# Optimization experiments

Hardware: AMD Instinct MI355X
Metric: run time of the kernel (lower is better)

## Reference

```python
import jax, jax.numpy as jnp
import numpy as np

N = 32768      # total nodes
E = 262144     # total edges (avg degree 8)
S = 128        # graph segments
B = 16         # batch entries
C = S // B     # segments per batch entry
NF, NC = 90, 36
OP, OD = 120, 64
D0, DX, GIN, GH = 190, 380, 256, 512


def setup_inputs() -> dict:
    key = jax.random.key(0)
    ks = jax.random.split(key, 16)
    rn = lambda k, shape, s=0.02: jax.random.normal(k, shape, jnp.float32) * s
    return {
        "node_features": jax.random.normal(ks[0], (N, NF), jnp.float32),
        "node_config_features": jax.random.normal(ks[1], (N, NC), jnp.float32),
        "emb_table": rn(ks[2], (OP, OD), 1.0),
        "w1": rn(ks[3], (DX, D0)), "b1": jnp.zeros((DX,), jnp.float32),
        "g1": jnp.ones((DX,), jnp.float32), "be1": jnp.zeros((DX,), jnp.float32),
        "w2": rn(ks[4], (GIN, DX)), "b2": jnp.zeros((GIN,), jnp.float32),
        "g2": jnp.ones((GIN,), jnp.float32), "be2": jnp.zeros((GIN,), jnp.float32),
        "wl1": rn(ks[5], (GH, GIN)), "bl1": jnp.zeros((GH,), jnp.float32), "wr1": rn(ks[6], (GH, GIN)),
        "wl2": rn(ks[7], (GH, GH)), "bl2": jnp.zeros((GH,), jnp.float32), "wr2": rn(ks[8], (GH, GH)),
        "wl3": rn(ks[9], (GH, GH)), "bl3": jnp.zeros((GH,), jnp.float32), "wr3": rn(ks[10], (GH, GH)),
        "wc": rn(ks[11], (1, GH)), "bc": jnp.zeros((1,), jnp.float32),
        "node_ops": jax.random.randint(ks[12], (N,), 0, OP),
        "edges": jax.random.randint(ks[13], (2, E), 0, N),
        # cumulative end indices, equal-size segments; batches = segment -> batch entry
        "node_separation": (jnp.arange(S, dtype=jnp.int32) + 1) * (N // S),
        "batches": jnp.repeat(jnp.arange(B, dtype=jnp.int32), C),
    }


def _leaky(x):
    return jnp.where(x >= 0, x, 0.01 * x)


def _graphwise_ln(x, seg_id, counts, gamma, beta):
    # per-graph-segment mean/var over all nodes and features, per-feature affine
    D = x.shape[1]
    s = jax.ops.segment_sum(jnp.sum(x, -1), seg_id, num_segments=S)
    ss = jax.ops.segment_sum(jnp.sum(x * x, -1), seg_id, num_segments=S)
    cnt = counts.astype(x.dtype) * D
    mean = s / cnt
    var = ss / cnt - mean * mean
    inv = jax.lax.rsqrt(var + 1e-5)
    return (x - mean[seg_id, None]) * inv[seg_id, None] * gamma + beta


def _pairnorm(x):
    # PyG PairNorm, scale=1: center over nodes, divide by sqrt(mean row norm^2)
    xc = x - jnp.mean(x, axis=0, keepdims=True)
    denom = 1e-5 + jnp.sqrt(jnp.mean(jnp.sum(xc * xc, -1)))
    return xc / denom


def _sage(x, src, dst, inv_deg, wl, bl, wr):
    # SAGEConv(mean): lin_l(mean_neighbors) + lin_r(x)
    agg = jax.ops.segment_sum(x[src], dst, num_segments=N) * inv_deg[:, None]
    return agg @ wl.T + bl + x @ wr.T


def reference(node_features, node_config_features, emb_table, w1, b1, g1, be1,
              w2, b2, g2, be2, wl1, bl1, wr1, wl2, bl2, wr2, wl3, bl3, wr3,
              wc, bc, node_ops, edges, node_separation, batches):
    seg_id = jnp.searchsorted(node_separation, jnp.arange(N), side="right")
    counts = jnp.diff(node_separation, prepend=0)
    src, dst = edges[0], edges[1]
    deg = jax.ops.segment_sum(jnp.ones((E,), jnp.float32), dst, num_segments=N)
    inv_deg = 1.0 / jnp.maximum(deg, 1.0)

    x = jnp.concatenate([node_features, node_config_features, emb_table[node_ops]], axis=1)
    # node_features_mlp: Linear -> LeakyReLU -> GLN -> Linear -> LeakyReLU -> GLN
    x = _graphwise_ln(_leaky(x @ w1.T + b1), seg_id, counts, g1, be1)
    x = _graphwise_ln(_leaky(x @ w2.T + b2), seg_id, counts, g2, be2)
    # GraphSAGE: 3 layers, PairNorm + ReLU after all but the last
    x = jax.nn.relu(_pairnorm(_sage(x, src, dst, inv_deg, wl1, bl1, wr1)))
    x = jax.nn.relu(_pairnorm(_sage(x, src, dst, inv_deg, wl2, bl2, wr2)))
    x = _sage(x, src, dst, inv_deg, wl3, bl3, wr3)
    # ragged per-segment sum pooling (replaces the python loop) -> [S, GH]
    seg_sums = jax.ops.segment_sum(x, seg_id, num_segments=S)
    # batches = repeat(arange(B), C) and segments are in order -> reshape groups
    agg = seg_sums.reshape(B, C, GH)
    out = agg @ wc.T + bc  # [B, C, 1]
    return jnp.squeeze(out, 2)
```

## Files before the change

kernel.cpp:

```cpp
#include <hip/hip_runtime.h>
#include <hip/hip_bf16.h>

#define NN   32768
#define EE   262144
#define SS   128
#define NF_  90
#define NC_  36
#define OD_  64
#define D0_  190
#define DX_  380
#define GIN_ 256
#define GH_  512

typedef __attribute__((ext_vector_type(8))) short  s8v;
typedef __attribute__((ext_vector_type(4))) float  f4v;

typedef const __attribute__((address_space(1))) void* gas_ptr;
typedef __attribute__((address_space(3))) void*       las_ptr;

__device__ __forceinline__ float bf2f(unsigned short u) {
  return __uint_as_float(((unsigned)u) << 16);
}
__device__ __forceinline__ unsigned short f2bf(float f) {
  unsigned u = __float_as_uint(f);
  u += 0x7FFFu + ((u >> 16) & 1u);
  return (unsigned short)(u >> 16);
}

__global__ void deg_count(const int* __restrict__ dst, int* __restrict__ deg) {
  int e = blockIdx.x * 256 + threadIdx.x;
  if (e < EE) atomicAdd(&deg[dst[e]], 1);
}

__global__ void inv_deg_k(const int* __restrict__ deg, float* __restrict__ inv_deg) {
  int n = blockIdx.x * 256 + threadIdx.x;
  if (n < NN) inv_deg[n] = 1.0f / fmaxf((float)deg[n], 1.0f);
}

__global__ __launch_bounds__(256) void blk_sum_k(const int* __restrict__ deg,
                                                 int* __restrict__ bsum) {
  __shared__ int buf[256];
  int tid = threadIdx.x;
  buf[tid] = deg[blockIdx.x * 256 + tid];
  __syncthreads();
  for (int off = 128; off > 0; off >>= 1) {
    if (tid < off) buf[tid] += buf[tid + off];
    __syncthreads();
  }
  if (tid == 0) bsum[blockIdx.x] = buf[0];
}

__global__ __launch_bounds__(128) void blk_scan_k(const int* __restrict__ bsum,
                                                  int* __restrict__ boff) {
  __shared__ int buf[128];
  int tid = threadIdx.x;
  int v = bsum[tid];
  buf[tid] = v;
  __syncthreads();
  for (int d = 1; d < 128; d <<= 1) {
    int t = (tid >= d) ? buf[tid - d] : 0;
    __syncthreads();
    if (tid >= d) buf[tid] += t;
    __syncthreads();
  }
  boff[tid] = buf[tid] - v;
}

__global__ __launch_bounds__(256) void offsets_k(const int* __restrict__ deg,
                                                 const int* __restrict__ boff,
                                                 int* __restrict__ offsets) {
  __shared__ int buf[256];
  int tid = threadIdx.x;
  int i = blockIdx.x * 256 + tid;
  int v = deg[i];
  buf[tid] = v;
  __syncthreads();
  for (int d = 1; d < 256; d <<= 1) {
    int t = (tid >= d) ? buf[tid - d] : 0;
    __syncthreads();
    if (tid >= d) buf[tid] += t;
    __syncthreads();
  }
  offsets[i] = boff[blockIdx.x] + buf[tid] - v;
  if (i == 0) offsets[NN] = EE;
}

__global__ void bucket_k(const int* __restrict__ src, const int* __restrict__ dst,
                         const int* __restrict__ offsets, int* __restrict__ cursor,
                         int* __restrict__ srcs) {
  int e = blockIdx.x * 256 + threadIdx.x;
  if (e < EE) {
    int d = dst[e];
    int pos = offsets[d] + atomicAdd(&cursor[d], 1);
    srcs[pos] = src[e];
  }
}

#define CW1  73728
#define CW2  172032
#define CWL1 303104
#define CWR1 434176
#define CWL2 696320
#define CWR2 958464
#define CWL3 1220608
#define CWR3 1482752

__global__ void conv_all(const float* __restrict__ w1, const float* __restrict__ w2,
                         const float* __restrict__ wl1, const float* __restrict__ wr1,
                         const float* __restrict__ wl2, const float* __restrict__ wr2,
                         const float* __restrict__ wl3, const float* __restrict__ wr3,
                         unsigned short* __restrict__ w1b, unsigned short* __restrict__ w2b,
                         unsigned short* __restrict__ wl1b, unsigned short* __restrict__ wr1b,
                         unsigned short* __restrict__ wl2b, unsigned short* __restrict__ wr2b,
                         unsigned short* __restrict__ wl3b, unsigned short* __restrict__ wr3b) {
  int idx = blockIdx.x * 256 + threadIdx.x;
  if (idx >= CWR3) return;
  if (idx < CW1) {
    int r = idx / 192, c = idx - r * 192;
    w1b[idx] = f2bf((r < DX_ && c < D0_) ? w1[r * D0_ + c] : 0.0f);
  } else if (idx < CW2) {
    int i = idx - CW1;
    int r = i / 384, c = i - r * 384;
    w2b[i] = f2bf((c < DX_) ? w2[r * DX_ + c] : 0.0f);
  } else if (idx < CWL1) { int i = idx - CW2;  wl1b[i] = f2bf(wl1[i]); }
  else if (idx < CWR1)   { int i = idx - CWL1; wr1b[i] = f2bf(wr1[i]); }
  else if (idx < CWL2)   { int i = idx - CWR1; wl2b[i] = f2bf(wl2[i]); }
  else if (idx < CWR2)   { int i = idx - CWL2; wr2b[i] = f2bf(wr2[i]); }
  else if (idx < CWL3)   { int i = idx - CWR2; wl3b[i] = f2bf(wl3[i]); }
  else                   { int i = idx - CWL3; wr3b[i] = f2bf(wr3[i]); }
}

__global__ void build_x0_bf16(const float* __restrict__ nf, const float* __restrict__ ncf,
                              const float* __restrict__ emb, const int* __restrict__ ops,
                              unsigned short* __restrict__ x0) {
  int idx = blockIdx.x * 256 + threadIdx.x;
  if (idx >= NN * 192) return;
  int n = idx / 192;
  int c = idx - n * 192;
  float v;
  if (c < NF_)            v = nf[n * NF_ + c];
  else if (c < NF_ + NC_) v = ncf[n * NC_ + (c - NF_)];
  else if (c < D0_)       v = emb[ops[n] * OD_ + (c - (NF_ + NC_))];
  else                    v = 0.0f;
  x0[idx] = f2bf(v);
}

__device__ __forceinline__ void stage_tile_async(const unsigned short* __restrict__ G, int ld,
                                                 int base_row, int k0,
                                                 unsigned short* __restrict__ lds, int tid) {
#pragma unroll
  for (int i = 0; i < 2; ++i) {
    int c = tid + i * 256;
    int row = c & 127;
    int off = c >> 7;
    const unsigned short* src = G + (size_t)(base_row + row) * ld + k0 + off * 8;
    unsigned short* dst = lds + off * 1024 + row * 8;
    __builtin_amdgcn_global_load_lds((gas_ptr)(const void*)src, (las_ptr)(void*)dst,
                                     16, 0, 0);
  }
}

__global__ __launch_bounds__(256) void mfma_gemm2(
    const unsigned short* __restrict__ A1, int lda1,
    const unsigned short* __restrict__ B1, int ldb1, int K1,
    const unsigned short* __restrict__ A2, int lda2,
    const unsigned short* __restrict__ B2, int ldb2, int K2,
    const float* __restrict__ bias,
    float* __restrict__ C, int ldc, int Nreal, int mode, int swz,
    float* __restrict__ st0, float* __restrict__ st1,
    const float* __restrict__ wcp, float* __restrict__ outp)
{
  __shared__ unsigned short As[4096];
  __shared__ unsigned short Bs[4096];
  __shared__ float red[256];
  __shared__ float cs[128], css[128];
  int tid = threadIdx.x;
  int lane = tid & 63;
  int w = tid >> 6;
  int wm = (w & 1) * 64;
  int wn = (w >> 1) * 64;
  int bm, bn;
  if (swz) {
    int L = blockIdx.x;
    int xcd = L & 7;
    int s = L >> 3;
    bn = (s & 3) * 128;
    bm = ((s >> 2) * 8 + xcd) * 128;
  } else {
    bm = blockIdx.y * 128;
    bn = blockIdx.x * 128;
  }
  int quad = lane >> 4;
  int r16 = lane & 15;

  f4v acc[4][4] = {};

#pragma unroll 1
  for (int ph = 0; ph < 2; ++ph) {
    const unsigned short* A = ph ? A2 : A1;
    const unsigned short* B = ph ? B2 : B1;
    int lda = ph ? lda2 : lda1;
    int ldb = ph ? ldb2 : ldb1;
    int K = ph ? K2 : K1;
    for (int k0 = 0; k0 < K; k0 += 32) {
      stage_tile_async(A, lda, bm, k0, As, tid);
      stage_tile_async(B, ldb, bn, k0, Bs, tid);
      __syncthreads();
      s8v af[4], bfr[4];
#pragma unroll
      for (int mi = 0; mi < 4; ++mi)
        af[mi] = *(const s8v*)&As[quad * 1024 + (wm + mi * 16 + r16) * 8];
#pragma unroll
      for (int ni = 0; ni < 4; ++ni)
        bfr[ni] = *(const s8v*)&Bs[quad * 1024 + (wn + ni * 16 + r16) * 8];
#pragma unroll
      for (int mi = 0; mi < 4; ++mi)
#pragma unroll
        for (int ni = 0; ni < 4; ++ni)
          acc[mi][ni] = __builtin_amdgcn_mfma_f32_16x16x32_bf16(
              af[mi], bfr[ni], acc[mi][ni], 0, 0, 0);
      __syncthreads();
    }
  }

  int seg = bm >> 8;

  if (mode == 1) {
    float lsum = 0.0f, lssq = 0.0f;
#pragma unroll
    for (int mi = 0; mi < 4; ++mi) {
      int gm = bm + wm + mi * 16 + quad * 4;
#pragma unroll
      for (int ni = 0; ni < 4; ++ni) {
        int gn = bn + wn + ni * 16 + r16;
        if (gn < Nreal) {
          float bv = bias[gn];
#pragma unroll
          for (int r = 0; r < 4; ++r) {
            float v = acc[mi][ni][r] + bv;
            v = (v >= 0.0f) ? v : 0.01f * v;
            C[(size_t)(gm + r) * ldc + gn] = v;
            lsum += v;
            lssq += v * v;
          }
        }
      }
    }
    red[tid] = lsum;
    __syncthreads();
    for (int off = 128; off > 0; off >>= 1) {
      if (tid < off) red[tid] += red[tid + off];
      __syncthreads();
    }
    if (tid == 0) atomicAdd(&st0[seg], red[0]);
    __syncthreads();
    red[tid] = lssq;
    __syncthreads();
    for (int off = 128; off > 0; off >>= 1) {
      if (tid < off) red[tid] += red[tid + off];
      __syncthreads();
    }
    if (tid == 0) atomicAdd(&st1[seg], red[0]);
  } else if (mode == 2) {
    if (tid < 128) { cs[tid] = 0.0f; css[tid] = 0.0f; }
    __syncthreads();
#pragma unroll
    for (int ni = 0; ni < 4; ++ni) {
      int col = wn + ni * 16 + r16;
      int gn = bn + col;
      float bv = bias[gn];
      float psum = 0.0f, pssq = 0.0f;
#pragma unroll
      for (int mi = 0; mi < 4; ++mi) {
        int gm = bm + wm + mi * 16 + quad * 4;
#pragma unroll
        for (int r = 0; r < 4; ++r) {
          float v = acc[mi][ni][r] + bv;
          C[(size_t)(gm + r) * ldc + gn] = v;
          psum += v;
          pssq += v * v;
        }
      }
      atomicAdd(&cs[col], psum);
      atomicAdd(&css[col], pssq);
    }
    __syncthreads();
    if (tid < 128) {
      atomicAdd(&st0[bn + tid], cs[tid]);
      atomicAdd(&st1[bn + tid], css[tid]);
    }
  } else {
    float part = 0.0f;
#pragma unroll
    for (int ni = 0; ni < 4; ++ni) {
      int gn = bn + wn + ni * 16 + r16;
      float bv = bias[gn];
      float wv = wcp[gn];
      float colsum = 0.0f;
#pragma unroll
      for (int mi = 0; mi < 4; ++mi)
#pragma unroll
        for (int r = 0; r < 4; ++r)
          colsum += acc[mi][ni][r] + bv;
      part += colsum * wv;
    }
    red[tid] = part;
    __syncthreads();
    for (int off = 128; off > 0; off >>= 1) {
      if (tid < off) red[tid] += red[tid + off];
      __syncthreads();
    }
    if (tid == 0) atomicAdd(&outp[seg], red[0]);
  }
}

__global__ __launch_bounds__(256) void gln_apply_bf16(
    const float* __restrict__ x, int ld, int D, int Dp,
    const float* __restrict__ seg_sum, const float* __restrict__ seg_ssq,
    const float* __restrict__ g, const float* __restrict__ be,
    unsigned short* __restrict__ out) {
  int r = blockIdx.x;
  int s = r >> 8;
  float cnt = 256.0f * (float)D;
  float m = seg_sum[s] / cnt;
  float var = seg_ssq[s] / cnt - m * m;
  float inv = rsqrtf(var + 1e-5f);
  const float* row = x + (size_t)r * ld;
  unsigned short* orow = out + (size_t)r * Dp;
  for (int c = threadIdx.x; c < Dp; c += 256) {
    float v = (c < D) ? ((row[c] - m) * inv * g[c] + be[c]) : 0.0f;
    orow[c] = f2bf(v);
  }
}

__global__ __launch_bounds__(256) void aggregate4(const unsigned short* __restrict__ x,
                                                  int D4log,
                                                  unsigned short* __restrict__ agg,
                                                  const int* __restrict__ offsets,
                                                  const int* __restrict__ srcs,
                                                  const float* __restrict__ inv_deg) {
  int tid = threadIdx.x;
  int D4 = 1 << D4log;
  int npb = 256 >> D4log;
  int n = blockIdx.x * npb + (tid >> D4log);
  int f4 = tid & (D4 - 1);
  int start = offsets[n], end = offsets[n + 1];
  float wgt = inv_deg[n];
  const uint2* xb = (const uint2*)x;
  float a0 = 0.0f, a1 = 0.0f, a2 = 0.0f, a3 = 0.0f;
  for (int e = start; e < end; ++e) {
    uint2 v = xb[((size_t)srcs[e] << D4log) + f4];
    a0 += bf2f((unsigned short)(v.x & 0xffffu));
    a1 += bf2f((unsigned short)(v.x >> 16));
    a2 += bf2f((unsigned short)(v.y & 0xffffu));
    a3 += bf2f((unsigned short)(v.y >> 16));
  }
  uint2 o;
  o.x = ((unsigned)f2bf(a1 * wgt) << 16) | (unsigned)f2bf(a0 * wgt);
  o.y = ((unsigned)f2bf(a3 * wgt) << 16) | (unsigned)f2bf(a2 * wgt);
  ((uint2*)agg)[((size_t)n << D4log) + f4] = o;
}

__global__ __launch_bounds__(512) void pn_finalize(const float* __restrict__ colsum,
                                                   const float* __restrict__ colssq,
                                                   float* __restrict__ mu,
                                                   float* __restrict__ invd) {
  int f = threadIdx.x;
  float m = colsum[f] / (float)NN;
  mu[f] = m;
  float t = colssq[f] / (float)NN - m * m;
  __shared__ float buf[512];
  buf[f] = t;
  __syncthreads();
  for (int off = 256; off > 0; off >>= 1) {
    if (f < off) buf[f] += buf[f + off];
    __syncthreads();
  }
  if (f == 0) invd[0] = 1.0f / (1e-5f + sqrtf(fmaxf(buf[0], 0.0f)));
}

__global__ __launch_bounds__(128) void pn_apply_v(const float* __restrict__ y,
                                                  const float* __restrict__ mu,
                                                  const float* __restrict__ invd,
                                                  unsigned short* __restrict__ xb) {
  int r = blockIdx.x;
  int f4 = threadIdx.x;
  float id = invd[0];
  float4 v = ((const float4*)(y + (size_t)r * GH_))[f4];
  float4 m = ((const float4*)mu)[f4];
  float v0 = fmaxf((v.x - m.x) * id, 0.0f);
  float v1 = fmaxf((v.y - m.y) * id, 0.0f);
  float v2 = fmaxf((v.z - m.z) * id, 0.0f);
  float v3 = fmaxf((v.w - m.w) * id, 0.0f);
  uint2 o;
  o.x = ((unsigned)f2bf(v1) << 16) | (unsigned)f2bf(v0);
  o.y = ((unsigned)f2bf(v3) << 16) | (unsigned)f2bf(v2);
  ((uint2*)(xb + (size_t)r * GH_))[f4] = o;
}

__global__ void init_out(float* __restrict__ out, const float* __restrict__ bc) {
  int s = threadIdx.x;
  if (s < SS) out[s] = bc[0];
}

extern "C" void kernel_launch(void* const* d_in, const int* in_sizes, int n_in,
                              void* d_out, int out_size, void* d_ws, size_t ws_size,
                              hipStream_t stream) {
  const float* node_features = (const float*)d_in[0];
  const float* node_config   = (const float*)d_in[1];
  const float* emb_table     = (const float*)d_in[2];
  const float* w1  = (const float*)d_in[3];
  const float* b1  = (const float*)d_in[4];
  const float* g1  = (const float*)d_in[5];
  const float* be1 = (const float*)d_in[6];
  const float* w2  = (const float*)d_in[7];
  const float* b2  = (const float*)d_in[8];
  const float* g2  = (const float*)d_in[9];
  const float* be2 = (const float*)d_in[10];
  const float* wl1 = (const float*)d_in[11];
  const float* bl1 = (const float*)d_in[12];
  const float* wr1 = (const float*)d_in[13];
  const float* wl2 = (const float*)d_in[14];
  const float* bl2 = (const float*)d_in[15];
  const float* wr2 = (const float*)d_in[16];
  const float* wl3 = (const float*)d_in[17];
  const float* bl3 = (const float*)d_in[18];
  const float* wr3 = (const float*)d_in[19];
  const float* wc  = (const float*)d_in[20];
  const float* bc  = (const float*)d_in[21];
  const int* node_ops = (const int*)d_in[22];
  const int* edges    = (const int*)d_in[23];
  float* out = (float*)d_out;

  char* ws = (char*)d_ws;
  size_t off = 0;
  auto alloc = [&](size_t bytes) -> void* {
    void* p = ws + off;
    off += (bytes + 255) & ~(size_t)255;
    return p;
  };

  int*   deg_i   = (int*)alloc(NN * 4);
  int*   cursor  = (int*)alloc(NN * 4);
  int*   offsets = (int*)alloc((NN + 1) * 4);
  int*   srcs    = (int*)alloc(EE * 4);
  int*   bsum    = (int*)alloc(SS * 4);
  int*   boff    = (int*)alloc(SS * 4);
  float* inv_deg = (float*)alloc(NN * 4);
  float* seg_sum = (float*)alloc(SS * 4);
  float* seg_ssq = (float*)alloc(SS * 4);
  float* colsum  = (float*)alloc(512 * 4);
  float* colssq  = (float*)alloc(512 * 4);
  float* mu      = (float*)alloc(512 * 4);
  float* invd    = (float*)alloc(256);
  unsigned short* w1b  = (unsigned short*)alloc((size_t)384 * 192 * 2);
  unsigned short* w2b  = (unsigned short*)alloc((size_t)256 * 384 * 2);
  unsigned short* wl1b = (unsigned short*)alloc((size_t)512 * 256 * 2);
  unsigned short* wr1b = (unsigned short*)alloc((size_t)512 * 256 * 2);
  unsigned short* wl2b = (unsigned short*)alloc((size_t)512 * 512 * 2);
  unsigned short* wr2b = (unsigned short*)alloc((size_t)512 * 512 * 2);
  unsigned short* wl3b = (unsigned short*)alloc((size_t)512 * 512 * 2);
  unsigned short* wr3b = (unsigned short*)alloc((size_t)512 * 512 * 2);
  float*          Y    = (float*)alloc((size_t)NN * 512 * 4);
  unsigned short* BF1  = (unsigned short*)alloc((size_t)NN * 512 * 2);
  unsigned short* BF2  = (unsigned short*)alloc((size_t)NN * 512 * 2);
  unsigned short* BF3  = (unsigned short*)alloc((size_t)NN * 512 * 2);

  const int* esrc = edges;
  const int* edst = edges + EE;

  hipMemsetAsync(deg_i, 0, NN * 4, stream);
  hipMemsetAsync(cursor, 0, NN * 4, stream);
  deg_count<<<EE / 256, 256, 0, stream>>>(edst, deg_i);
  blk_sum_k<<<NN / 256, 256, 0, stream>>>(deg_i, bsum);
  blk_scan_k<<<1, 128, 0, stream>>>(bsum, boff);
  offsets_k<<<NN / 256, 256, 0, stream>>>(deg_i, boff, offsets);
  inv_deg_k<<<NN / 256, 256, 0, stream>>>(deg_i, inv_deg);
  bucket_k<<<EE / 256, 256, 0, stream>>>(esrc, edst, offsets, cursor, srcs);

  conv_all<<<(CWR3 + 255) / 256, 256, 0, stream>>>(w1, w2, wl1, wr1, wl2, wr2, wl3, wr3,
                                                   w1b, w2b, wl1b, wr1b, wl2b, wr2b,
                                                   wl3b, wr3b);

  init_out<<<1, SS, 0, stream>>>(out, bc);

  build_x0_bf16<<<(NN * 192 + 255) / 256, 256, 0, stream>>>(node_features, node_config,
                                                            emb_table, node_ops, BF1);
  hipMemsetAsync(seg_sum, 0, 1024, stream);
  {
    dim3 g(384 / 128, NN / 128);
    mfma_gemm2<<<g, 256, 0, stream>>>(BF1, 192, w1b, 192, 192,
                                      nullptr, 0, nullptr, 0, 0,
                                      b1, Y, 384, DX_, 1, 0,
                                      seg_sum, seg_ssq, nullptr, nullptr);
  }
  gln_apply_bf16<<<NN, 256, 0, stream>>>(Y, 384, DX_, 384, seg_sum, seg_ssq, g1, be1, BF2);

  hipMemsetAsync(seg_sum, 0, 1024, stream);
  {
    dim3 g(256 / 128, NN / 128);
    mfma_gemm2<<<g, 256, 0, stream>>>(BF2, 384, w2b, 384, 384,
                                      nullptr, 0, nullptr, 0, 0,
                                      b2, Y, 256, GIN_, 1, 0,
                                      seg_sum, seg_ssq, nullptr, nullptr);
  }
  gln_apply_bf16<<<NN, 256, 0, stream>>>(Y, 256, GIN_, 256, seg_sum, seg_ssq, g2, be2, BF3);

  aggregate4<<<NN / 4, 256, 0, stream>>>(BF3, 6, BF1, offsets, srcs, inv_deg);
  hipMemsetAsync(colsum, 0, 4096, stream);
  mfma_gemm2<<<1024, 256, 0, stream>>>(BF1, 256, wl1b, 256, 256,
                                       BF3, 256, wr1b, 256, 256,
                                       bl1, Y, 512, GH_, 2, 1,
                                       colsum, colssq, nullptr, nullptr);
  pn_finalize<<<1, 512, 0, stream>>>(colsum, colssq, mu, invd);
  pn_apply_v<<<NN, 128, 0, stream>>>(Y, mu, invd, BF2);

  aggregate4<<<NN / 2, 256, 0, stream>>>(BF2, 7, BF1, offsets, srcs, inv_deg);
  hipMemsetAsync(colsum, 0, 4096, stream);
  mfma_gemm2<<<1024, 256, 0, stream>>>(BF1, 512, wl2b, 512, 512,
                                       BF2, 512, wr2b, 512, 512,
                                       bl2, Y, 512, GH_, 2, 1,
                                       colsum, colssq, nullptr, nullptr);
  pn_finalize<<<1, 512, 0, stream>>>(colsum, colssq, mu, invd);
  pn_apply_v<<<NN, 128, 0, stream>>>(Y, mu, invd, BF3);

  aggregate4<<<NN / 2, 256, 0, stream>>>(BF3, 7, BF1, offsets, srcs, inv_deg);
  mfma_gemm2<<<1024, 256, 0, stream>>>(BF1, 512, wl3b, 512, 512,
                                       BF3, 512, wr3b, 512, 512,
                                       bl3, nullptr, 512, GH_, 3, 1,
                                       nullptr, nullptr, wc, out);
}
```

Before: 663.7 us.

## Merge prep kernels and memsets, widen aggregation to 16-byte loads, reuse LDS

Merges weight conversion, input building, output init and stat zeroing into one grid-stride prep kernel. The inverse-degree computation moves into the offsets kernel, and the two degree/cursor memsets become one, assuming the two buffers are contiguous. The neighbour aggregation now loads eight bf16 values per thread as uint4 instead of four, and the GEMM reuses its staging LDS for the reduction scratch, which cuts LDS use. These changes mainly remove launches and memsets and reduce gather instruction count, at the cost of relying on buffer adjacency.

```diff
diff --git a/kernel.cpp b/kernel.cpp
--- a/kernel.cpp
+++ b/kernel.cpp
@@ -18,23 +18,21 @@
 typedef const __attribute__((address_space(1))) void* gas_ptr;
 typedef __attribute__((address_space(3))) void*       las_ptr;
 
-__device__ __forceinline__ float bf2f(unsigned short u) {
-  return __uint_as_float(((unsigned)u) << 16);
+__device__ __forceinline__ float bf2f(unsigned u) {
+  return __uint_as_float(u << 16);
 }
 __device__ __forceinline__ unsigned short f2bf(float f) {
   unsigned u = __float_as_uint(f);
   u += 0x7FFFu + ((u >> 16) & 1u);
   return (unsigned short)(u >> 16);
 }
+__device__ __forceinline__ unsigned pack2(float a, float b) {
+  return ((unsigned)f2bf(b) << 16) | (unsigned)f2bf(a);
+}
 
 __global__ void deg_count(const int* __restrict__ dst, int* __restrict__ deg) {
   int e = blockIdx.x * 256 + threadIdx.x;
   if (e < EE) atomicAdd(&deg[dst[e]], 1);
-}
-
-__global__ void inv_deg_k(const int* __restrict__ deg, float* __restrict__ inv_deg) {
-  int n = blockIdx.x * 256 + threadIdx.x;
-  if (n < NN) inv_deg[n] = 1.0f / fmaxf((float)deg[n], 1.0f);
 }
 
 __global__ __launch_bounds__(256) void blk_sum_k(const int* __restrict__ deg,
@@ -68,7 +66,8 @@
 
 __global__ __launch_bounds__(256) void offsets_k(const int* __restrict__ deg,
                                                  const int* __restrict__ boff,
-                                                 int* __restrict__ offsets) {
+                                                 int* __restrict__ offsets,
+                                                 float* __restrict__ inv_deg) {
   __shared__ int buf[256];
   int tid = threadIdx.x;
   int i = blockIdx.x * 256 + tid;
@@ -82,6 +81,7 @@
     __syncthreads();
   }
   offsets[i] = boff[blockIdx.x] + buf[tid] - v;
+  inv_deg[i] = 1.0f / fmaxf((float)v, 1.0f);
   if (i == 0) offsets[NN] = EE;
 }
 
@@ -105,44 +105,50 @@
 #define CWL3 1220608
 #define CWR3 1482752
 
-__global__ void conv_all(const float* __restrict__ w1, const float* __restrict__ w2,
-                         const float* __restrict__ wl1, const float* __restrict__ wr1,
-                         const float* __restrict__ wl2, const float* __restrict__ wr2,
-                         const float* __restrict__ wl3, const float* __restrict__ wr3,
-                         unsigned short* __restrict__ w1b, unsigned short* __restrict__ w2b,
-                         unsigned short* __restrict__ wl1b, unsigned short* __restrict__ wr1b,
-                         unsigned short* __restrict__ wl2b, unsigned short* __restrict__ wr2b,
-                         unsigned short* __restrict__ wl3b, unsigned short* __restrict__ wr3b) {
-  int idx = blockIdx.x * 256 + threadIdx.x;
-  if (idx >= CWR3) return;
-  if (idx < CW1) {
-    int r = idx / 192, c = idx - r * 192;
-    w1b[idx] = f2bf((r < DX_ && c < D0_) ? w1[r * D0_ + c] : 0.0f);
-  } else if (idx < CW2) {
-    int i = idx - CW1;
-    int r = i / 384, c = i - r * 384;
-    w2b[i] = f2bf((c < DX_) ? w2[r * DX_ + c] : 0.0f);
-  } else if (idx < CWL1) { int i = idx - CW2;  wl1b[i] = f2bf(wl1[i]); }
-  else if (idx < CWR1)   { int i = idx - CWL1; wr1b[i] = f2bf(wr1[i]); }
-  else if (idx < CWL2)   { int i = idx - CWR1; wl2b[i] = f2bf(wl2[i]); }
-  else if (idx < CWR2)   { int i = idx - CWL2; wr2b[i] = f2bf(wr2[i]); }
-  else if (idx < CWL3)   { int i = idx - CWR2; wl3b[i] = f2bf(wl3[i]); }
-  else                   { int i = idx - CWL3; wr3b[i] = f2bf(wr3[i]); }
-}
-
-__global__ void build_x0_bf16(const float* __restrict__ nf, const float* __restrict__ ncf,
-                              const float* __restrict__ emb, const int* __restrict__ ops,
-                              unsigned short* __restrict__ x0) {
-  int idx = blockIdx.x * 256 + threadIdx.x;
-  if (idx >= NN * 192) return;
-  int n = idx / 192;
-  int c = idx - n * 192;
-  float v;
-  if (c < NF_)            v = nf[n * NF_ + c];
-  else if (c < NF_ + NC_) v = ncf[n * NC_ + (c - NF_)];
-  else if (c < D0_)       v = emb[ops[n] * OD_ + (c - (NF_ + NC_))];
-  else                    v = 0.0f;
-  x0[idx] = f2bf(v);
+__global__ __launch_bounds__(256) void prep_all(
+    const float* __restrict__ nf, const float* __restrict__ ncf,
+    const float* __restrict__ emb, const int* __restrict__ ops,
+    const float* __restrict__ w1, const float* __restrict__ w2,
+    const float* __restrict__ wl1, const float* __restrict__ wr1,
+    const float* __restrict__ wl2, const float* __restrict__ wr2,
+    const float* __restrict__ wl3, const float* __restrict__ wr3,
+    unsigned short* __restrict__ w1b, unsigned short* __restrict__ w2b,
+    unsigned short* __restrict__ wl1b, unsigned short* __restrict__ wr1b,
+    unsigned short* __restrict__ wl2b, unsigned short* __restrict__ wr2b,
+    unsigned short* __restrict__ wl3b, unsigned short* __restrict__ wr3b,
+    unsigned short* __restrict__ x0,
+    float* __restrict__ stat_all, float* __restrict__ outp,
+    const float* __restrict__ bc)
+{
+  const int T = 4096 * 256;
+  int gidx = blockIdx.x * 256 + threadIdx.x;
+  for (int i = gidx; i < 2560; i += T) stat_all[i] = 0.0f;
+  if (gidx < SS) outp[gidx] = bc[0];
+  for (int i = gidx; i < CWR3; i += T) {
+    if (i < CW1) {
+      int r = i / 192, c = i - r * 192;
+      w1b[i] = f2bf((r < DX_ && c < D0_) ? w1[r * D0_ + c] : 0.0f);
+    } else if (i < CW2) {
+      int j = i - CW1;
+      int r = j / 384, c = j - r * 384;
+      w2b[j] = f2bf((c < DX_) ? w2[r * DX_ + c] : 0.0f);
+    } else if (i < CWL1) { int j = i - CW2;  wl1b[j] = f2bf(wl1[j]); }
+    else if (i < CWR1)   { int j = i - CWL1; wr1b[j] = f2bf(wr1[j]); }
+    else if (i < CWL2)   { int j = i - CWR1; wl2b[j] = f2bf(wl2[j]); }
+    else if (i < CWR2)   { int j = i - CWL2; wr2b[j] = f2bf(wr2[j]); }
+    else if (i < CWL3)   { int j = i - CWR2; wl3b[j] = f2bf(wl3[j]); }
+    else                 { int j = i - CWL3; wr3b[j] = f2bf(wr3[j]); }
+  }
+  for (int i = gidx; i < NN * 192; i += T) {
+    int n = i / 192;
+    int c = i - n * 192;
+    float v;
+    if (c < NF_)            v = nf[n * NF_ + c];
+    else if (c < NF_ + NC_) v = ncf[n * NC_ + (c - NF_)];
+    else if (c < D0_)       v = emb[ops[n] * OD_ + (c - (NF_ + NC_))];
+    else                    v = 0.0f;
+    x0[i] = f2bf(v);
+  }
 }
 
 __device__ __forceinline__ void stage_tile_async(const unsigned short* __restrict__ G, int ld,
@@ -172,8 +178,6 @@
 {
   __shared__ unsigned short As[4096];
   __shared__ unsigned short Bs[4096];
-  __shared__ float red[256];
-  __shared__ float cs[128], css[128];
   int tid = threadIdx.x;
   int lane = tid & 63;
   int w = tid >> 6;
@@ -222,6 +226,10 @@
       __syncthreads();
     }
   }
+
+  float* red = (float*)As;
+  float* cs  = (float*)Bs;
+  float* css = ((float*)Bs) + 128;
 
   int seg = bm >> 8;
 
@@ -333,32 +341,32 @@
   }
 }
 
-__global__ __launch_bounds__(256) void aggregate4(const unsigned short* __restrict__ x,
-                                                  int D4log,
+__global__ __launch_bounds__(256) void aggregate8(const unsigned short* __restrict__ x,
+                                                  int L8,
                                                   unsigned short* __restrict__ agg,
                                                   const int* __restrict__ offsets,
                                                   const int* __restrict__ srcs,
                                                   const float* __restrict__ inv_deg) {
   int tid = threadIdx.x;
-  int D4 = 1 << D4log;
-  int npb = 256 >> D4log;
-  int n = blockIdx.x * npb + (tid >> D4log);
-  int f4 = tid & (D4 - 1);
+  int n = (blockIdx.x << (8 - L8)) + (tid >> L8);
+  int f8 = tid & ((1 << L8) - 1);
   int start = offsets[n], end = offsets[n + 1];
   float wgt = inv_deg[n];
-  const uint2* xb = (const uint2*)x;
-  float a0 = 0.0f, a1 = 0.0f, a2 = 0.0f, a3 = 0.0f;
+  const uint4* xb = (const uint4*)x;
+  float a0 = 0, a1 = 0, a2 = 0, a3 = 0, a4 = 0, a5 = 0, a6 = 0, a7 = 0;
   for (int e = start; e < end; ++e) {
-    uint2 v = xb[((size_t)srcs[e] << D4log) + f4];
-    a0 += bf2f((unsigned short)(v.x & 0xffffu));
-    a1 += bf2f((unsigned short)(v.x >> 16));
-    a2 += bf2f((unsigned short)(v.y & 0xffffu));
-    a3 += bf2f((unsigned short)(v.y >> 16));
-  }
-  uint2 o;
-  o.x = ((unsigned)f2bf(a1 * wgt) << 16) | (unsigned)f2bf(a0 * wgt);
-  o.y = ((unsigned)f2bf(a3 * wgt) << 16) | (unsigned)f2bf(a2 * wgt);
-  ((uint2*)agg)[((size_t)n << D4log) + f4] = o;
+    uint4 v = xb[((size_t)srcs[e] << L8) + f8];
+    a0 += bf2f(v.x & 0xffffu); a1 += bf2f(v.x >> 16);
+    a2 += bf2f(v.y & 0xffffu); a3 += bf2f(v.y >> 16);
+    a4 += bf2f(v.z & 0xffffu); a5 += bf2f(v.z >> 16);
+    a6 += bf2f(v.w & 0xffffu); a7 += bf2f(v.w >> 16);
+  }
+  uint4 o;
+  o.x = pack2(a0 * wgt, a1 * wgt);
+  o.y = pack2(a2 * wgt, a3 * wgt);
+  o.z = pack2(a4 * wgt, a5 * wgt);
+  o.w = pack2(a6 * wgt, a7 * wgt);
+  ((uint4*)agg)[((size_t)n << L8) + f8] = o;
 }
 
 __global__ __launch_bounds__(512) void pn_finalize(const float* __restrict__ colsum,
@@ -393,14 +401,9 @@
   float v2 = fmaxf((v.z - m.z) * id, 0.0f);
   float v3 = fmaxf((v.w - m.w) * id, 0.0f);
   uint2 o;
-  o.x = ((unsigned)f2bf(v1) << 16) | (unsigned)f2bf(v0);
-  o.y = ((unsigned)f2bf(v3) << 16) | (unsigned)f2bf(v2);
+  o.x = pack2(v0, v1);
+  o.y = pack2(v2, v3);
   ((uint2*)(xb + (size_t)r * GH_))[f4] = o;
-}
-
-__global__ void init_out(float* __restrict__ out, const float* __restrict__ bc) {
-  int s = threadIdx.x;
-  if (s < SS) out[s] = bc[0];
 }
 
 extern "C" void kernel_launch(void* const* d_in, const int* in_sizes, int n_in,
@@ -447,10 +450,7 @@
   int*   bsum    = (int*)alloc(SS * 4);
   int*   boff    = (int*)alloc(SS * 4);
   float* inv_deg = (float*)alloc(NN * 4);
-  float* seg_sum = (float*)alloc(SS * 4);
-  float* seg_ssq = (float*)alloc(SS * 4);
-  float* colsum  = (float*)alloc(512 * 4);
-  float* colssq  = (float*)alloc(512 * 4);
+  float* stat_all= (float*)alloc(2560 * 4);
   float* mu      = (float*)alloc(512 * 4);
   float* invd    = (float*)alloc(256);
   unsigned short* w1b  = (unsigned short*)alloc((size_t)384 * 192 * 2);
@@ -469,62 +469,59 @@
   const int* esrc = edges;
   const int* edst = edges + EE;
 
-  hipMemsetAsync(deg_i, 0, NN * 4, stream);
-  hipMemsetAsync(cursor, 0, NN * 4, stream);
+  float* gln1s = stat_all;       float* gln1q = stat_all + 128;
+  float* gln2s = stat_all + 256; float* gln2q = stat_all + 384;
+  float* pn1s  = stat_all + 512; float* pn1q  = stat_all + 1024;
+  float* pn2s  = stat_all + 1536; float* pn2q = stat_all + 2048;
+
+  hipMemsetAsync(deg_i, 0, (size_t)NN * 4 * 2, stream);
+
   deg_count<<<EE / 256, 256, 0, stream>>>(edst, deg_i);
   blk_sum_k<<<NN / 256, 256, 0, stream>>>(deg_i, bsum);
   blk_scan_k<<<1, 128, 0, stream>>>(bsum, boff);
-  offsets_k<<<NN / 256, 256, 0, stream>>>(deg_i, boff, offsets);
-  inv_deg_k<<<NN / 256, 256, 0, stream>>>(deg_i, inv_deg);
+  offsets_k<<<NN / 256, 256, 0, stream>>>(deg_i, boff, offsets, inv_deg);
   bucket_k<<<EE / 256, 256, 0, stream>>>(esrc, edst, offsets, cursor, srcs);
 
-  conv_all<<<(CWR3 + 255) / 256, 256, 0, stream>>>(w1, w2, wl1, wr1, wl2, wr2, wl3, wr3,
-                                                   w1b, w2b, wl1b, wr1b, wl2b, wr2b,
-                                                   wl3b, wr3b);
-
-  init_out<<<1, SS, 0, stream>>>(out, bc);
-
-  build_x0_bf16<<<(NN * 192 + 255) / 256, 256, 0, stream>>>(node_features, node_config,
-                                                            emb_table, node_ops, BF1);
-  hipMemsetAsync(seg_sum, 0, 1024, stream);
+  prep_all<<<4096, 256, 0, stream>>>(node_features, node_config, emb_table, node_ops,
+                                     w1, w2, wl1, wr1, wl2, wr2, wl3, wr3,
+                                     w1b, w2b, wl1b, wr1b, wl2b, wr2b, wl3b, wr3b,
+                                     BF1, stat_all, out, bc);
+
   {
-    dim3 g(384 / 128, NN / 128);
+    dim3 g(3, 256);
     mfma_gemm2<<<g, 256, 0, stream>>>(BF1, 192, w1b, 192, 192,
                                       nullptr, 0, nullptr, 0, 0,
                                       b1, Y, 384, DX_, 1, 0,
-                                      seg_sum, seg_ssq, nullptr, nullptr);
-  }
-  gln_apply_bf16<<<NN, 256, 0, stream>>>(Y, 384, DX_, 384, seg_sum, seg_ssq, g1, be1, BF2);
-
-  hipMemsetAsync(seg_sum, 0, 1024, stream);
+                                      gln1s, gln1q, nullptr, nullptr);
+  }
+  gln_apply_bf16<<<NN, 256, 0, stream>>>(Y, 384, DX_, 384, gln1s, gln1q, g1, be1, BF2);
+
   {
-    dim3 g(256 / 128, NN / 128);
+    dim3 g(2, 256);
     mfma_gemm2<<<g, 256, 0, stream>>>(BF2, 384, w2b, 384, 384,
                                       nullptr, 0, nullptr, 0, 0,
                                       b2, Y, 256, GIN_, 1, 0,
-                                      seg_sum, seg_ssq, nullptr, nullptr);
-  }
-  gln_apply_bf16<<<NN, 256, 0, stream>>>(Y, 256, GIN_, 256, seg_sum, seg_ssq, g2, be2, BF3);
-
-  aggregate4<<<NN / 4, 256, 0, stream>>>(BF3, 6, BF1, offsets, srcs, inv_deg);
-  hipMemsetAsync(colsum, 0, 4096, stream);
+                                      gln2s, gln2q, nullptr, nullptr);
+  }
+  gln_apply_bf16<<<NN, 256, 0, stream>>>(Y, 256, GIN_, 256, gln2s, gln2q, g2, be2, BF3);
+
+  aggregate8<<<NN / 8, 256, 0, stream>>>(BF3, 5, BF1, offsets, srcs, inv_deg);
   mfma_gemm2<<<1024, 256, 0, stream>>>(BF1, 256, wl1b, 256, 256,
                                        BF3, 256, wr1b, 256, 256,
                                        bl1, Y, 512, GH_, 2, 1,
-                                       colsum, colssq, nullptr, nullptr);
-  pn_finalize<<<1, 512, 0, stream>>>(colsum, colssq, mu, invd);
+                                       pn1s, pn1q, nullptr, nullptr);
+  pn_finalize<<<1, 512, 0, stream>>>(pn1s, pn1q, mu, invd);
   pn_apply_v<<<NN, 128, 0, stream>>>(Y, mu, invd, BF2);
 
-  aggregate4<<<NN / 2, 256, 0, stream>>>(BF2, 7, BF1, offsets, srcs, inv_deg);
-  hipMemsetAsync(colsum, 0, 4096, stream);
+  aggregate8<<<NN / 4, 256, 0, stream>>>(BF2, 6, BF1, offsets, srcs, inv_deg);
   mfma_gemm2<<<1024, 256, 0, stream>>>(BF1, 512, wl2b, 512, 512,
                                        BF2, 512, wr2b, 512, 512,
                                        bl2, Y, 512, GH_, 2, 1,
-                                       colsum, colssq, nullptr, nullptr);
-  pn_finalize<<<1, 512, 0, stream>>>(colsum, colssq, mu, invd);
+                                       pn2s, pn2q, nullptr, nullptr);
+  pn_finalize<<<1, 512, 0, stream>>>(pn2s, pn2q, mu, invd);
   pn_apply_v<<<NN, 128, 0, stream>>>(Y, mu, invd, BF3);
 
-  aggregate4<<<NN / 2, 256, 0, stream>>>(BF3, 7, BF1, offsets, srcs, inv_deg);
+  aggregate8<<<NN / 4, 256, 0, stream>>>(BF3, 6, BF1, offsets, srcs, inv_deg);
   mfma_gemm2<<<1024, 256, 0, stream>>>(BF1, 512, wl3b, 512, 512,
                                        BF3, 512, wr3b, 512, 512,
                                        bl3, nullptr, 512, GH_, 3, 1,
```

Measured after the change: 601.6 us. -9.4%, faster.
